# Performance work log

Hardware: AMD Instinct MI355X
Metric: run time of the kernel (lower is better)

The kernel has to match this reference:

```python
import math
import jax, jax.numpy as jnp
import numpy as np

B, S, D, H, DK, DV = 4, 2048, 512, 8, 64, 64

def setup_inputs() -> dict:
    key = jax.random.key(0)
    ks = jax.random.split(key, 6)
    x = jax.random.normal(ks[0], (B, S, D), jnp.float32)
    W_Q = jax.random.normal(ks[1], (H, D, DK), jnp.float32) / D
    W_K = jax.random.normal(ks[2], (H, D, DK), jnp.float32) / D
    W_V = jax.random.normal(ks[3], (H, D, DV), jnp.float32) / D
    W_G = jax.random.normal(ks[4], (D, H * DV), jnp.float32) / D
    W_O = jax.random.normal(ks[5], (H * DV, D), jnp.float32) / D
    return {"x": x, "W_Q": W_Q, "W_K": W_K, "W_V": W_V, "W_G": W_G, "W_O": W_O}

def _decay_matrix(n_heads, seq_len, dtype):
    # gammas per head, exactly as in __init__
    gammas = 1.0 - jnp.exp(jnp.linspace(math.log(1.0 / 32), math.log(1.0 / 512), n_heads))
    n = jnp.arange(seq_len)
    diff = n[:, None] - n[None, :]                      # [S,S]
    mask = diff >= 0
    safe = jnp.where(mask, diff, 0)
    dec = jnp.where(mask[None], gammas[:, None, None].astype(dtype) ** safe[None], 0.0)
    return dec                                           # [H,S,S]

def reference(x, W_Q, W_K, W_V, W_G, W_O):
    Bx, Sx, Dx = x.shape
    Hn = W_Q.shape[0]
    dv = W_V.shape[-1]
    # per-head projections (all heads vectorized)
    Q = jnp.einsum('bsd,hdk->bhsk', x, W_Q)
    K = jnp.einsum('bsd,hdk->bhsk', x, W_K)
    V = jnp.einsum('bsd,hdv->bhsv', x, W_V)
    Dmat = _decay_matrix(Hn, Sx, x.dtype)                # [H,S,S] causal decay
    # retention scores: QK^T elementwise-weighted by decay (no softmax)
    A = jnp.einsum('bhsk,bhtk->bhst', Q, K) * Dmat[None]  # [B,H,S,S] == self_retentions
    ret = jnp.einsum('bhst,bhtv->bhsv', A, V)            # [B,H,S,dv]
    out_heads = ret.transpose(0, 2, 1, 3).reshape(Bx, Sx, Hn * dv)  # concat over heads
    # GroupNorm(num_groups=H, num_channels=H) applied to reshape(-1, H):
    # each group has exactly 1 element -> mean == x, var == 0 -> output is 0.
    eps = 1e-5
    flat = out_heads.reshape(-1, Hn)
    mean = flat
    var = jnp.zeros_like(flat)
    Y = ((flat - mean) * jax.lax.rsqrt(var + eps)).reshape(out_heads.shape)
    # swish-gated output projection
    g = x @ W_G
    out = (g * jax.nn.sigmoid(g) * Y) @ W_O              # [B,S,D]
    return out, A
```

## Files before the change

kernel.cpp:

```cpp
#include <hip/hip_runtime.h>
#include <hip/hip_bf16.h>
#include <math.h>

#define B_ 4
#define S_ 2048
#define D_ 512
#define H_ 8
#define DK_ 64

typedef __bf16 bf16x8 __attribute__((ext_vector_type(8)));
typedef float f32x16 __attribute__((ext_vector_type(16)));
typedef float f32x4 __attribute__((ext_vector_type(4)));

static __device__ __forceinline__ unsigned short f2bf(float f) {
    unsigned int u = __builtin_bit_cast(unsigned int, f);
    unsigned int r = (u + 0x7FFFu + ((u >> 16) & 1u)) >> 16;
    return (unsigned short)r;
}

__global__ __launch_bounds__(256) void k_setup(const float* __restrict__ wq, const float* __restrict__ wk,
                                               unsigned short* __restrict__ wqT, unsigned short* __restrict__ wkT,
                                               float* __restrict__ tab) {
    const int bx = blockIdx.x;
    if (bx < 2048) {
        int idx = bx * 256 + threadIdx.x;
        const int n = H_ * DK_ * D_;
        const float* src = idx < n ? wq : wk;
        unsigned short* dst = idx < n ? wqT : wkT;
        int o = idx < n ? idx : idx - n;
        int d  = o % D_;
        int hk = o / D_;
        int k  = hk % DK_;
        int h  = hk / DK_;
        dst[o] = f2bf(src[(h * D_ + d) * DK_ + k]);
    } else {
        int i = (bx - 2048) * 256 + threadIdx.x;
        if (i < H_ * S_) {
            int h = i / S_;
            int n = i % S_;
            double xv = -3.4657359027997265 - (double)h * (2.772588722239781 / 7.0);
            double g = 1.0 - exp(xv);
            tab[i] = (float)pow(g, (double)n);
        }
    }
}

__global__ __launch_bounds__(256, 2) void k_proj(const float* __restrict__ x,
                                                 const unsigned short* __restrict__ wqT,
                                                 const unsigned short* __restrict__ wkT,
                                                 unsigned short* __restrict__ qb,
                                                 unsigned short* __restrict__ kb) {
    const int tid  = threadIdx.x;
    const int lane = tid & 63;
    const int wave = tid >> 6;
    const int m0   = blockIdx.x * 32;
    const int half = blockIdx.y;
    const unsigned short* wt = half ? wkT : wqT;
    unsigned short* outp     = half ? kb  : qb;

    __shared__ unsigned short atile[32 * 520];

    {
        const float4* xsrc = reinterpret_cast<const float4*>(x + (size_t)m0 * D_);
#pragma unroll
        for (int i = 0; i < 16; ++i) {
            int u   = tid + i * 256;
            int row = u >> 7, c4 = u & 127;
            float4 v = xsrc[u];
            ushort4 o;
            o.x = f2bf(v.x); o.y = f2bf(v.y); o.z = f2bf(v.z); o.w = f2bf(v.w);
            *reinterpret_cast<ushort4*>(&atile[row * 520 + c4 * 4]) = o;
        }
    }
    __syncthreads();

    const int row  = lane & 31;
    const int col  = lane & 31;
    const int hi   = lane >> 5;
    const int koff = hi * 8;
    const int n0   = wave * 128;

    const unsigned short* b0 = wt + (size_t)(n0 +  0 + row) * D_ + koff;
    const unsigned short* b1 = wt + (size_t)(n0 + 32 + row) * D_ + koff;
    const unsigned short* b2 = wt + (size_t)(n0 + 64 + row) * D_ + koff;
    const unsigned short* b3 = wt + (size_t)(n0 + 96 + row) * D_ + koff;
    const unsigned short* ap = atile + row * 520 + koff;

    f32x16 acc0 = {}, acc1 = {}, acc2 = {}, acc3 = {};
#pragma unroll
    for (int kk = 0; kk < D_; kk += 16) {
        bf16x8 a = *reinterpret_cast<const bf16x8*>(ap + kk);
        acc0 = __builtin_amdgcn_mfma_f32_32x32x16_bf16(a, *reinterpret_cast<const bf16x8*>(b0 + kk), acc0, 0, 0, 0);
        acc1 = __builtin_amdgcn_mfma_f32_32x32x16_bf16(a, *reinterpret_cast<const bf16x8*>(b1 + kk), acc1, 0, 0, 0);
        acc2 = __builtin_amdgcn_mfma_f32_32x32x16_bf16(a, *reinterpret_cast<const bf16x8*>(b2 + kk), acc2, 0, 0, 0);
        acc3 = __builtin_amdgcn_mfma_f32_32x32x16_bf16(a, *reinterpret_cast<const bf16x8*>(b3 + kk), acc3, 0, 0, 0);
    }

#define EPI(ACC, NB) { \
    int n = n0 + (NB) * 32 + col; \
    int hh = n >> 6, k = n & 63; \
    _Pragma("unroll") \
    for (int r = 0; r < 16; ++r) { \
        int rowD = (r & 3) + 8 * (r >> 2) + 4 * hi; \
        int m = m0 + rowD; \
        int bidx = m >> 11, s = m & 2047; \
        outp[(((size_t)bidx * H_ + hh) * S_ + s) * DK_ + k] = f2bf(ACC[r]); \
    } }
    EPI(acc0, 0) EPI(acc1, 1) EPI(acc2, 2) EPI(acc3, 3)
#undef EPI
}

static __device__ __forceinline__ void fill_step(int bid, int i, int tid,
        float* __restrict__ aout, float* __restrict__ out0) {
    f32x4 z = {0.f, 0.f, 0.f, 0.f};
    if (i < 7) {
        const int f = bid * 7 + i;
        const int bh = f / 112;
        int r = f % 112;
        int g = 0, cum = 0;
        for (; g < 7; ++g) { int cnt = 4 * (7 - g); if (r < cum + cnt) break; cum += cnt; }
        const int rr  = r - cum;
        const int per = 7 - g;
        const int panel = g * 4 + rr / per;
        const int st    = g + 1 + rr % per;
        float* base = aout + (size_t)bh * S_ * S_ + (size_t)(panel * 64) * S_ + st * 256;
#pragma unroll
        for (int j = 0; j < 16; ++j) {
            int u = tid + j * 256;
            *reinterpret_cast<f32x4*>(base + (size_t)(u >> 6) * S_ + (u & 63) * 4) = z;
        }
    } else {
        f32x4* b0 = reinterpret_cast<f32x4*>(out0) + (size_t)bid * 2048;
#pragma unroll
        for (int j = 0; j < 8; ++j)
            b0[tid + j * 256] = z;
    }
}

__global__ __launch_bounds__(256) void k_scorefill(const unsigned short* __restrict__ qb,
                                                   const unsigned short* __restrict__ kb,
                                                   const float* __restrict__ tab,
                                                   float* __restrict__ aout,
                                                   float* __restrict__ out0) {
    __shared__ __align__(16) float tile[64 * 256];
    const int id  = blockIdx.x;
    const int tid = threadIdx.x;
    const int lane = tid & 63;
    const int w    = tid >> 6;
    const int c    = id & 7, sidx = id >> 3;
    const int bh   = (c >> 1) + 4 * (sidx >> 3);
    const int p    = ((sidx & 7) << 1) | (c & 1);
    const int h    = bh & (H_ - 1);
    float* ablk = aout + (size_t)bh * S_ * S_;
    const float* th = tab + h * S_;

    const int col  = lane & 31;
    const int hi   = lane >> 5;
    const int koff = hi * 8;

    const float c1 = 1.0f / th[col];
    float grc[16];
    int rowDv[16];
#pragma unroll
    for (int r = 0; r < 16; ++r) {
        rowDv[r] = (r & 3) + 8 * (r >> 2) + 4 * hi;
        grc[r] = th[rowDv[r]] * c1;
    }

    int fillIdx = 0;

    for (int pp = 0; pp < 2; ++pp) {
        const int panel = pp ? (31 - p) : p;
        const int s0 = panel * 64;
        const int qq = panel >> 2;
        const int rb = panel & 3;

        bf16x8 qf[2][4];
#pragma unroll
        for (int rg = 0; rg < 2; ++rg) {
            const unsigned short* qp = qb + ((size_t)bh * S_ + s0 + rg * 32 + col) * DK_ + koff;
#pragma unroll
            for (int i = 0; i < 4; ++i)
                qf[rg][i] = *reinterpret_cast<const bf16x8*>(qp + 16 * i);
        }

        for (int st = 0; st <= qq; ++st) {
            if (fillIdx < 8) { fill_step(id, fillIdx, tid, aout, out0); ++fillIdx; }

            const int t0 = st * 256;
            const int ct0 = t0 + w * 64;
            const bool active = (st < qq) || (w <= rb);
            if (active) {
                f32x16 acc[2][2] = {{{}, {}}, {{}, {}}};
#pragma unroll
                for (int cg = 0; cg < 2; ++cg) {
                    const unsigned short* kp = kb + ((size_t)bh * S_ + ct0 + cg * 32 + col) * DK_ + koff;
                    bf16x8 kf0 = *reinterpret_cast<const bf16x8*>(kp);
                    bf16x8 kf1 = *reinterpret_cast<const bf16x8*>(kp + 16);
                    bf16x8 kf2 = *reinterpret_cast<const bf16x8*>(kp + 32);
                    bf16x8 kf3 = *reinterpret_cast<const bf16x8*>(kp + 48);
#pragma unroll
                    for (int rg = 0; rg < 2; ++rg) {
                        acc[rg][cg] = __builtin_amdgcn_mfma_f32_32x32x16_bf16(qf[rg][0], kf0, acc[rg][cg], 0, 0, 0);
                        acc[rg][cg] = __builtin_amdgcn_mfma_f32_32x32x16_bf16(qf[rg][1], kf1, acc[rg][cg], 0, 0, 0);
                        acc[rg][cg] = __builtin_amdgcn_mfma_f32_32x32x16_bf16(qf[rg][2], kf2, acc[rg][cg], 0, 0, 0);
                        acc[rg][cg] = __builtin_amdgcn_mfma_f32_32x32x16_bf16(qf[rg][3], kf3, acc[rg][cg], 0, 0, 0);
                    }
                }
                if (st < qq || w < rb) {
#pragma unroll
                    for (int rg = 0; rg < 2; ++rg) {
#pragma unroll
                        for (int cg = 0; cg < 2; ++cg) {
                            const float sc = th[s0 + rg * 32 - ct0 - cg * 32];
#pragma unroll
                            for (int r = 0; r < 16; ++r)
                                tile[(rg * 32 + rowDv[r]) * 256 + w * 64 + cg * 32 + col] =
                                    acc[rg][cg][r] * grc[r] * sc;
                        }
                    }
                } else {
#pragma unroll
                    for (int rg = 0; rg < 2; ++rg) {
#pragma unroll
                        for (int cg = 0; cg < 2; ++cg) {
                            const int dbase = 32 * (rg - cg);
#pragma unroll
                            for (int r = 0; r < 16; ++r) {
                                int d = dbase + rowDv[r] - col;
                                float v = (d >= 0) ? acc[rg][cg][r] * th[d] : 0.0f;
                                tile[(rg * 32 + rowDv[r]) * 256 + w * 64 + cg * 32 + col] = v;
                            }
                        }
                    }
                }
            } else {
                f32x4 z = {0.f, 0.f, 0.f, 0.f};
#pragma unroll
                for (int i = 0; i < 16; ++i) {
                    int r = i * 4 + (lane >> 4);
                    int cc = (lane & 15) * 4;
                    *reinterpret_cast<f32x4*>(&tile[r * 256 + w * 64 + cc]) = z;
                }
            }
            __syncthreads();
#pragma unroll
            for (int r = 0; r < 16; ++r) {
                int row = w * 16 + r;
                f32x4 v = *reinterpret_cast<const f32x4*>(&tile[row * 256 + lane * 4]);
                *reinterpret_cast<f32x4*>(ablk + (size_t)(s0 + row) * S_ + t0 + lane * 4) = v;
            }
            __syncthreads();
        }
    }
}

extern "C" void kernel_launch(void* const* d_in, const int* in_sizes, int n_in,
                              void* d_out, int out_size, void* d_ws, size_t ws_size,
                              hipStream_t stream) {
    const float* x  = (const float*)d_in[0];
    const float* wq = (const float*)d_in[1];
    const float* wk = (const float*)d_in[2];

    char* ws = (char*)d_ws;
    unsigned short* wqT = (unsigned short*)(ws);
    unsigned short* wkT = (unsigned short*)(ws + 524288);
    unsigned short* qb  = (unsigned short*)(ws + 1048576);
    unsigned short* kb  = (unsigned short*)(ws + 9437184);
    float*          tab = (float*)(ws + 17825792);

    float* out0 = (float*)d_out;
    float* aout = (float*)d_out + (size_t)B_ * S_ * D_;

    hipLaunchKernelGGL(k_setup, dim3(2112), dim3(256), 0, stream,
                       wq, wk, wqT, wkT, tab);
    hipLaunchKernelGGL(k_proj, dim3(B_*S_/32, 2), dim3(256), 0, stream,
                       x, wqT, wkT, qb, kb);
    hipLaunchKernelGGL(k_scorefill, dim3(512), dim3(256), 0, stream,
                       qb, kb, tab, aout, out0);
}
```

Baseline: 165.3 us.

## Reblock projection weights and stage Q/K outputs through LDS for coalesced stores

The transposed bf16 weights are now stored in a k-blocked layout of 8 elements per row, so each lane's 16-byte B-operand loads are contiguous across lanes. The projection kernel computes both Q and K in one block, reusing the x tile already converted into LDS, which halves the x reads. Accumulators go to an LDS output tile and are then written to global memory as coalesced 16-byte vectors instead of scattered 2-byte stores. In exchange it adds extra LDS (two 32x520 tiles), which may lower occupancy, plus extra barriers, and it launches half as many blocks.

```diff
diff --git a/kernel.cpp b/kernel.cpp
--- a/kernel.cpp
+++ b/kernel.cpp
@@ -19,20 +19,20 @@
 }
 
 __global__ __launch_bounds__(256) void k_setup(const float* __restrict__ wq, const float* __restrict__ wk,
-                                               unsigned short* __restrict__ wqT, unsigned short* __restrict__ wkT,
+                                               unsigned short* __restrict__ wqT2, unsigned short* __restrict__ wkT2,
                                                float* __restrict__ tab) {
     const int bx = blockIdx.x;
     if (bx < 2048) {
         int idx = bx * 256 + threadIdx.x;
         const int n = H_ * DK_ * D_;
         const float* src = idx < n ? wq : wk;
-        unsigned short* dst = idx < n ? wqT : wkT;
+        unsigned short* dst = idx < n ? wqT2 : wkT2;
         int o = idx < n ? idx : idx - n;
         int d  = o % D_;
         int hk = o / D_;
+        int h  = hk / DK_;
         int k  = hk % DK_;
-        int h  = hk / DK_;
-        dst[o] = f2bf(src[(h * D_ + d) * DK_ + k]);
+        dst[(((size_t)(d >> 3) * 512 + hk) << 3) + (d & 7)] = f2bf(src[(h * D_ + d) * DK_ + k]);
     } else {
         int i = (bx - 2048) * 256 + threadIdx.x;
         if (i < H_ * S_) {
@@ -46,19 +46,19 @@
 }
 
 __global__ __launch_bounds__(256, 2) void k_proj(const float* __restrict__ x,
-                                                 const unsigned short* __restrict__ wqT,
-                                                 const unsigned short* __restrict__ wkT,
+                                                 const unsigned short* __restrict__ wqT2,
+                                                 const unsigned short* __restrict__ wkT2,
                                                  unsigned short* __restrict__ qb,
                                                  unsigned short* __restrict__ kb) {
     const int tid  = threadIdx.x;
     const int lane = tid & 63;
     const int wave = tid >> 6;
     const int m0   = blockIdx.x * 32;
-    const int half = blockIdx.y;
-    const unsigned short* wt = half ? wkT : wqT;
-    unsigned short* outp     = half ? kb  : qb;
+    const int bidx = m0 >> 11;
+    const int s0   = m0 & 2047;
 
     __shared__ unsigned short atile[32 * 520];
+    __shared__ unsigned short otile[32 * 520];
 
     {
         const float4* xsrc = reinterpret_cast<const float4*>(x + (size_t)m0 * D_);
@@ -74,40 +74,53 @@
     }
     __syncthreads();
 
-    const int row  = lane & 31;
-    const int col  = lane & 31;
-    const int hi   = lane >> 5;
-    const int koff = hi * 8;
-    const int n0   = wave * 128;
-
-    const unsigned short* b0 = wt + (size_t)(n0 +  0 + row) * D_ + koff;
-    const unsigned short* b1 = wt + (size_t)(n0 + 32 + row) * D_ + koff;
-    const unsigned short* b2 = wt + (size_t)(n0 + 64 + row) * D_ + koff;
-    const unsigned short* b3 = wt + (size_t)(n0 + 96 + row) * D_ + koff;
-    const unsigned short* ap = atile + row * 520 + koff;
-
-    f32x16 acc0 = {}, acc1 = {}, acc2 = {}, acc3 = {};
-#pragma unroll
-    for (int kk = 0; kk < D_; kk += 16) {
-        bf16x8 a = *reinterpret_cast<const bf16x8*>(ap + kk);
-        acc0 = __builtin_amdgcn_mfma_f32_32x32x16_bf16(a, *reinterpret_cast<const bf16x8*>(b0 + kk), acc0, 0, 0, 0);
-        acc1 = __builtin_amdgcn_mfma_f32_32x32x16_bf16(a, *reinterpret_cast<const bf16x8*>(b1 + kk), acc1, 0, 0, 0);
-        acc2 = __builtin_amdgcn_mfma_f32_32x32x16_bf16(a, *reinterpret_cast<const bf16x8*>(b2 + kk), acc2, 0, 0, 0);
-        acc3 = __builtin_amdgcn_mfma_f32_32x32x16_bf16(a, *reinterpret_cast<const bf16x8*>(b3 + kk), acc3, 0, 0, 0);
-    }
-
-#define EPI(ACC, NB) { \
+    const int col = lane & 31;
+    const int hi  = lane >> 5;
+    const int n0  = wave * 128;
+    const unsigned short* ap = atile + col * 520 + hi * 8;
+
+    for (int half = 0; half < 2; ++half) {
+        const unsigned short* wt = half ? wkT2 : wqT2;
+        unsigned short* outp     = half ? kb  : qb;
+
+        f32x16 acc0 = {}, acc1 = {}, acc2 = {}, acc3 = {};
+        const unsigned short* bp0 = wt + hi * 4096 + (size_t)(n0 + col) * 8;
+#pragma unroll 8
+        for (int ks = 0; ks < 32; ++ks) {
+            bf16x8 a = *reinterpret_cast<const bf16x8*>(ap + ks * 16);
+            const unsigned short* bp = bp0 + ks * 8192;
+            acc0 = __builtin_amdgcn_mfma_f32_32x32x16_bf16(a, *reinterpret_cast<const bf16x8*>(bp),        acc0, 0, 0, 0);
+            acc1 = __builtin_amdgcn_mfma_f32_32x32x16_bf16(a, *reinterpret_cast<const bf16x8*>(bp + 256),  acc1, 0, 0, 0);
+            acc2 = __builtin_amdgcn_mfma_f32_32x32x16_bf16(a, *reinterpret_cast<const bf16x8*>(bp + 512),  acc2, 0, 0, 0);
+            acc3 = __builtin_amdgcn_mfma_f32_32x32x16_bf16(a, *reinterpret_cast<const bf16x8*>(bp + 768),  acc3, 0, 0, 0);
+        }
+
+        if (half) __syncthreads();
+
+#define EPO(ACC, NB) { \
     int n = n0 + (NB) * 32 + col; \
-    int hh = n >> 6, k = n & 63; \
     _Pragma("unroll") \
     for (int r = 0; r < 16; ++r) { \
         int rowD = (r & 3) + 8 * (r >> 2) + 4 * hi; \
-        int m = m0 + rowD; \
-        int bidx = m >> 11, s = m & 2047; \
-        outp[(((size_t)bidx * H_ + hh) * S_ + s) * DK_ + k] = f2bf(ACC[r]); \
+        otile[rowD * 520 + n] = f2bf(ACC[r]); \
     } }
-    EPI(acc0, 0) EPI(acc1, 1) EPI(acc2, 2) EPI(acc3, 3)
-#undef EPI
+        EPO(acc0, 0) EPO(acc1, 1) EPO(acc2, 2) EPO(acc3, 3)
+#undef EPO
+        __syncthreads();
+
+#pragma unroll
+        for (int i = 0; i < 8; ++i) {
+            int u    = tid + i * 256;
+            int head = u >> 8;
+            int v    = u & 255;
+            int s    = v >> 3;
+            int kc   = v & 7;
+            f32x4 val = *reinterpret_cast<const f32x4*>(&otile[s * 520 + head * 64 + kc * 8]);
+            unsigned short* dst = outp + (((size_t)(bidx * H_ + head) * S_ + s0 + s) * DK_) + kc * 8;
+            *reinterpret_cast<f32x4*>(dst) = val;
+        }
+        if (!half) __syncthreads();
+    }
 }
 
 static __device__ __forceinline__ void fill_step(int bid, int i, int tid,
@@ -263,19 +276,19 @@
     const float* wk = (const float*)d_in[2];
 
     char* ws = (char*)d_ws;
-    unsigned short* wqT = (unsigned short*)(ws);
-    unsigned short* wkT = (unsigned short*)(ws + 524288);
-    unsigned short* qb  = (unsigned short*)(ws + 1048576);
-    unsigned short* kb  = (unsigned short*)(ws + 9437184);
-    float*          tab = (float*)(ws + 17825792);
+    unsigned short* wqT2 = (unsigned short*)(ws);
+    unsigned short* wkT2 = (unsigned short*)(ws + 524288);
+    unsigned short* qb   = (unsigned short*)(ws + 1048576);
+    unsigned short* kb   = (unsigned short*)(ws + 9437184);
+    float*          tab  = (float*)(ws + 17825792);
 
     float* out0 = (float*)d_out;
     float* aout = (float*)d_out + (size_t)B_ * S_ * D_;
 
     hipLaunchKernelGGL(k_setup, dim3(2112), dim3(256), 0, stream,
-                       wq, wk, wqT, wkT, tab);
-    hipLaunchKernelGGL(k_proj, dim3(B_*S_/32, 2), dim3(256), 0, stream,
-                       x, wqT, wkT, qb, kb);
+                       wq, wk, wqT2, wkT2, tab);
+    hipLaunchKernelGGL(k_proj, dim3(B_*S_/32), dim3(256), 0, stream,
+                       x, wqT2, wkT2, qb, kb);
     hipLaunchKernelGGL(k_scorefill, dim3(512), dim3(256), 0, stream,
                        qb, kb, tab, aout, out0);
 }
```

Result: slower. 173.4 us (+4.9%).
